# Kernel tuning notes

Measured on AMD Instinct MI355X. Metric: run time of the kernel, lower is better.

Reference implementation:

```python
import jax, jax.numpy as jnp
import numpy as np

B, S, H = 2, 2048, 2048
NH, G = 16, 4
HD = H // NH          # 128
REP = NH // G         # 4 query heads per KV group
KV = G * HD           # 512


def setup_inputs() -> dict:
    key = jax.random.key(0)
    ks = jax.random.split(key, 10)
    s = 0.02
    X = jax.random.normal(ks[0], (B, S, H), dtype=jnp.float32)
    Wq = jax.random.normal(ks[1], (H, H), dtype=jnp.float32) * s
    bq = jnp.zeros((H,), dtype=jnp.float32)
    Wk = jax.random.normal(ks[2], (H, KV), dtype=jnp.float32) * s
    bk = jnp.zeros((KV,), dtype=jnp.float32)
    Wv = jax.random.normal(ks[3], (H, KV), dtype=jnp.float32) * s
    bv = jnp.zeros((KV,), dtype=jnp.float32)
    Wo = jax.random.normal(ks[4], (H, H), dtype=jnp.float32) * s
    bo = jnp.zeros((H,), dtype=jnp.float32)
    # causal mask: 1 where attention is disallowed (strict upper triangle)
    casual_mask = jnp.triu(jnp.ones((S, S), dtype=jnp.float32), k=1)[None, None]
    return {"X": X, "Wq": Wq, "bq": bq, "Wk": Wk, "bk": bk,
            "Wv": Wv, "bv": bv, "Wo": Wo, "bo": bo,
            "casual_mask": casual_mask}


def reference(X, Wq, bq, Wk, bk, Wv, bv, Wo, bo, casual_mask):
    # projections
    q = X @ Wq + bq                          # [B,S,H]
    k = X @ Wk + bk                          # [B,S,G*HD]
    v = X @ Wv + bv                          # [B,S,G*HD]
    # split heads; q grouped as (group, rep) to match torch expand ordering
    q = q.reshape(B, S, NH, HD).transpose(0, 2, 1, 3)       # [B,NH,S,HD]
    q = q.reshape(B, G, REP, S, HD)                          # [B,G,REP,S,HD]
    k = k.reshape(B, S, G, HD).transpose(0, 2, 1, 3)         # [B,G,S,HD]
    v = v.reshape(B, S, G, HD).transpose(0, 2, 1, 3)         # [B,G,S,HD]
    scale = 1.0 / jnp.sqrt(jnp.float32(HD))
    scores = jnp.einsum('bgrqd,bgkd->bgrqk', q, k) * scale   # [B,G,REP,S,S]
    scores = scores + casual_mask * (-1e9)
    probs = jax.nn.softmax(scores, axis=-1)
    out = jnp.einsum('bgrqk,bgkd->bgrqd', probs, v)          # [B,G,REP,S,HD]
    out = out.reshape(B, NH, S, HD).transpose(0, 2, 1, 3).reshape(B, S, H)
    return out @ Wo + bo
```

## Files before the change

### kernel.cpp

```cpp
#include <hip/hip_runtime.h>

#define B_   2
#define S_   2048
#define H_   2048
#define NH_  16
#define G_   4
#define HD_  128
#define KV_  512
#define HQKV 3072

typedef __attribute__((ext_vector_type(8))) short bf16x8;
typedef __attribute__((ext_vector_type(4))) float f32x4;

__device__ __forceinline__ unsigned short f2bf(float f) {
    unsigned u = __float_as_uint(f);
    u += 0x7fff + ((u >> 16) & 1);
    return (unsigned short)(u >> 16);
}
__device__ __forceinline__ float bf2f(unsigned short s) {
    return __uint_as_float(((unsigned)s) << 16);
}
__device__ __forceinline__ unsigned cvtpk(float a, float b) {
    unsigned r;
    asm volatile("v_cvt_pk_bf16_f32 %0, %1, %2" : "=v"(r) : "v"(a), "v"(b));
    return r;
}

#define GLDS16(gsrc, ldst)                                                            \
    __builtin_amdgcn_global_load_lds(                                                 \
        (const __attribute__((address_space(1))) void*)(gsrc),                        \
        (__attribute__((address_space(3))) void*)(ldst), 16, 0, 0)

#define SC2F (0.08838834764831843f * 1.4426950408889634f)

__global__ void k_cvt_bf16(const float* __restrict__ in, unsigned short* __restrict__ out, int n4) {
    int i = blockIdx.x * blockDim.x + threadIdx.x;
    if (i >= n4) return;
    float4 v = ((const float4*)in)[i];
    ushort4 o;
    o.x = f2bf(v.x); o.y = f2bf(v.y); o.z = f2bf(v.z); o.w = f2bf(v.w);
    ((ushort4*)out)[i] = o;
}

__global__ void k_transpose_cvt(const float* __restrict__ in, unsigned short* __restrict__ out,
                                int R, int C) {
    __shared__ float t[32][33];
    int c0 = blockIdx.x * 32, r0 = blockIdx.y * 32;
    int tx = threadIdx.x, ty = threadIdx.y;
#pragma unroll
    for (int i = 0; i < 4; ++i)
        t[ty + i*8][tx] = in[(size_t)(r0 + ty + i*8) * C + c0 + tx];
    __syncthreads();
#pragma unroll
    for (int i = 0; i < 4; ++i)
        out[(size_t)(c0 + ty + i*8) * R + r0 + tx] = f2bf(t[tx][ty + i*8]);
}

__global__ void k_transpose_qkv(const float* __restrict__ Wq, const float* __restrict__ Wk,
                                const float* __restrict__ Wv, unsigned short* __restrict__ out) {
    __shared__ float t[32][33];
    int n0g = blockIdx.x * 32;
    int h0 = blockIdx.y * 32;
    const float* src; int C, n0l;
    if (n0g < H_)            { src = Wq; C = H_;  n0l = n0g; }
    else if (n0g < H_ + KV_) { src = Wk; C = KV_; n0l = n0g - H_; }
    else                     { src = Wv; C = KV_; n0l = n0g - H_ - KV_; }
    int tx = threadIdx.x, ty = threadIdx.y;
#pragma unroll
    for (int i = 0; i < 4; ++i)
        t[ty + i*8][tx] = src[(size_t)(h0 + ty + i*8) * C + n0l + tx];
    __syncthreads();
#pragma unroll
    for (int i = 0; i < 4; ++i)
        out[(size_t)(n0g + ty + i*8) * H_ + h0 + tx] = f2bf(t[tx][ty + i*8]);
}

__global__ void k_concat_bias(const float* __restrict__ bq, const float* __restrict__ bk,
                              const float* __restrict__ bv, float* __restrict__ out) {
    int i = blockIdx.x * 256 + threadIdx.x;
    if (i >= HQKV) return;
    out[i] = (i < H_) ? bq[i] : (i < H_ + KV_ ? bk[i - H_] : bv[i - H_ - KV_]);
}

__global__ void k_transpose_v(const unsigned short* __restrict__ in, unsigned short* __restrict__ out) {
    __shared__ unsigned short t[32][33];
    int b = blockIdx.z;
    int c0 = blockIdx.x * 32, s0 = blockIdx.y * 32;
    int tx = threadIdx.x, ty = threadIdx.y;
#pragma unroll
    for (int i = 0; i < 4; ++i)
        t[ty + i*8][tx] = in[((size_t)b * S_ + s0 + ty + i*8) * HQKV + (H_ + KV_) + c0 + tx];
    __syncthreads();
#pragma unroll
    for (int i = 0; i < 4; ++i)
        out[((size_t)b * KV_ + c0 + ty + i*8) * S_ + s0 + tx] = t[tx][ty + i*8];
}

template <bool BF16OUT, bool QSCALE>
__global__ __launch_bounds__(256) void k_gemm_bt(
    const unsigned short* __restrict__ A, const unsigned short* __restrict__ Bt,
    const float* __restrict__ bias, void* __restrict__ Cout, int M, int N, int K) {
    __shared__ __align__(16) unsigned short As[128 * 64];
    __shared__ __align__(16) unsigned short Bs[128 * 64];
    const int tid = threadIdx.x, lane = tid & 63, w = tid >> 6;
    const int l15 = lane & 15, l4 = lane >> 4;
    const int wr = w >> 1, wc = w & 1;
    const int m0 = blockIdx.x * 128, n0 = blockIdx.y * 128;
    f32x4 acc[4][4] = {};

    for (int kt = 0; kt < K; kt += 64) {
        __syncthreads();
#pragma unroll
        for (int i = 0; i < 4; ++i) {
            int p = (w * 4 + i) * 64 + lane;
            int row = p >> 3, c = (p & 7) ^ (row & 7);
            GLDS16(A + (size_t)(m0 + row) * K + kt + c * 8, As + (size_t)(w * 4 + i) * 512);
        }
#pragma unroll
        for (int i = 0; i < 4; ++i) {
            int p = (w * 4 + i) * 64 + lane;
            int row = p >> 3, c = (p & 7) ^ (row & 7);
            GLDS16(Bt + (size_t)(n0 + row) * K + kt + c * 8, Bs + (size_t)(w * 4 + i) * 512);
        }
        __syncthreads();
#pragma unroll
        for (int ks = 0; ks < 2; ++ks) {
            bf16x8 af[4], bfr[4];
#pragma unroll
            for (int m = 0; m < 4; ++m) {
                int row = wr * 64 + m * 16 + l15;
                int ch = (ks * 4 + l4) ^ (row & 7);
                af[m] = *(const bf16x8*)(As + row * 64 + ch * 8);
            }
#pragma unroll
            for (int n = 0; n < 4; ++n) {
                int row = wc * 64 + n * 16 + l15;
                int ch = (ks * 4 + l4) ^ (row & 7);
                bfr[n] = *(const bf16x8*)(Bs + row * 64 + ch * 8);
            }
#pragma unroll
            for (int m = 0; m < 4; ++m)
#pragma unroll
                for (int n = 0; n < 4; ++n)
                    acc[m][n] = __builtin_amdgcn_mfma_f32_16x16x32_bf16(af[m], bfr[n], acc[m][n], 0, 0, 0);
        }
    }
#pragma unroll
    for (int m = 0; m < 4; ++m) {
        int row = m0 + wr * 64 + m * 16 + l4 * 4;
#pragma unroll
        for (int n = 0; n < 4; ++n) {
            int col = n0 + wc * 64 + n * 16 + l15;
            float bv = bias[col];
#pragma unroll
            for (int r = 0; r < 4; ++r) {
                float v = acc[m][n][r] + bv;
                if (QSCALE) { if (col < H_) v *= SC2F; }
                if (BF16OUT)
                    ((unsigned short*)Cout)[(size_t)(row + r) * N + col] = f2bf(v);
                else
                    ((float*)Cout)[(size_t)(row + r) * N + col] = v;
            }
        }
    }
}

__global__ __launch_bounds__(256, 4) void k_flash(
    const unsigned short* __restrict__ QKV,
    const unsigned short* __restrict__ VT,
    unsigned short* __restrict__ Oa,
    unsigned short* __restrict__ part1,
    float* __restrict__ mlbuf) {
    __shared__ __align__(16) unsigned short Ks[64 * 128];
    __shared__ __align__(16) unsigned short Vs[128 * 64];
    const int tid = threadIdx.x, lane = tid & 63, w = tid >> 6;
    const int l15 = lane & 15, l4 = lane >> 4;
    const int bid = blockIdx.x;
    const int xcd = bid & 7, idx = bid >> 3;
    const int bh = xcd * 4 + (idx & 3);
    const int jidx = idx >> 2;
    const int b = bh >> 4, nh = bh & 15, g = nh >> 2;

    int qt, t0, t1, mode;
    if (jidx < 16) { qt = 16 + jidx; t0 = 0; t1 = 16; mode = 1; }
    else {
        int k = jidx - 16, j = k >> 1;
        if ((k & 1) == 0) { qt = 31 - j; t0 = 16; t1 = qt + 1; mode = 2; }
        else              { qt = 15 - j; t0 = 0;  t1 = qt + 1; mode = 0; }
    }
    const int qbase = qt * 64 + w * 16;

    const unsigned short* kgbase = QKV + (size_t)b * S_ * HQKV + H_ + g * HD_;
    const unsigned short* vgbase = VT + ((size_t)b * KV_ + g * HD_) * S_;

    auto issueK = [&](int kt) {
        const int kv0 = kt * 64;
#pragma unroll
        for (int i = 0; i < 4; ++i) {
            int p = i * 256 + tid;
            int row = p >> 4, c = (p & 15) ^ (row & 15);
            GLDS16(kgbase + (size_t)(kv0 + row) * HQKV + c * 8, &Ks[(i * 256 + w * 64) * 8]);
        }
    };
    auto issueV = [&](int kt) {
        const int kv0 = kt * 64;
#pragma unroll
        for (int i = 0; i < 4; ++i) {
            int p = i * 256 + tid;
            int row = p >> 3, c = (p & 7) ^ (row & 7);
            GLDS16(vgbase + (size_t)row * S_ + kv0 + c * 8, &Vs[(i * 256 + w * 64) * 8]);
        }
    };

    bf16x8 qf[4];
#pragma unroll
    for (int kb = 0; kb < 4; ++kb)
        qf[kb] = *(const bf16x8*)(QKV + (size_t)(b * S_ + qbase + l15) * HQKV +
                                  nh * HD_ + kb * 32 + l4 * 8);

    f32x4 o[8] = {};
    float m_r = -1e30f, l_r = 0.f;

    const int src0 = l15 + 16 * ((2 * l4) & 3);
    const int src1 = l15 + 16 * ((2 * l4 + 1) & 3);
    const bool hsel = ((l4 >> 1) & 1) != 0;

    issueK(t0);
    issueV(t0);

    for (int kt = t0; kt < t1; ++kt) {
        const int kv0 = kt * 64;
        asm volatile("s_waitcnt vmcnt(4)" ::: "memory");
        __builtin_amdgcn_s_barrier();
        __builtin_amdgcn_sched_barrier(0);

        f32x4 s[4] = {};
#pragma unroll
        for (int kb = 0; kb < 4; ++kb) {
            bf16x8 kf[4];
#pragma unroll
            for (int n = 0; n < 4; ++n) {
                int row = n * 16 + l15;
                int sl = (kb * 4 + l4) ^ (row & 15);
                kf[n] = *(const bf16x8*)(&Ks[(row * 16 + sl) * 8]);
            }
            __builtin_amdgcn_s_setprio(1);
#pragma unroll
            for (int n = 0; n < 4; ++n)
                s[n] = __builtin_amdgcn_mfma_f32_16x16x32_bf16(kf[n], qf[kb], s[n], 0, 0, 0);
            __builtin_amdgcn_s_setprio(0);
        }
        if (kv0 + 63 > qbase) {
            const int qrow = qbase + l15;
#pragma unroll
            for (int n = 0; n < 4; ++n)
#pragma unroll
                for (int r = 0; r < 4; ++r) {
                    int kcol = kv0 + n * 16 + l4 * 4 + r;
                    if (kcol > qrow) s[n][r] = -1e30f;
                }
        }
        float pmax = s[0][0];
#pragma unroll
        for (int n = 0; n < 4; ++n)
#pragma unroll
            for (int r = 0; r < 4; ++r) pmax = fmaxf(pmax, s[n][r]);
        pmax = fmaxf(pmax, __shfl_xor(pmax, 16));
        pmax = fmaxf(pmax, __shfl_xor(pmax, 32));
        if (__any(pmax > m_r + 8.0f)) {
            float mn = fmaxf(m_r, pmax);
            float sf = exp2f(m_r - mn);
            m_r = mn;
            l_r *= sf;
#pragma unroll
            for (int nc = 0; nc < 8; ++nc) {
                f32x4 t = o[nc];
                t[0] *= sf; t[1] *= sf; t[2] *= sf; t[3] *= sf;
                o[nc] = t;
            }
        }
        float rsum = 0.f;
#pragma unroll
        for (int n = 0; n < 4; ++n)
#pragma unroll
            for (int r = 0; r < 4; ++r) {
                float p = exp2f(s[n][r] - m_r);
                s[n][r] = p;
                rsum += p;
            }
        rsum += __shfl_xor(rsum, 16);
        rsum += __shfl_xor(rsum, 32);
        l_r += rsum;

        unsigned plo[4], phi[4];
#pragma unroll
        for (int n = 0; n < 4; ++n) {
            plo[n] = cvtpk(s[n][0], s[n][1]);
            phi[n] = cvtpk(s[n][2], s[n][3]);
        }

        asm volatile("s_waitcnt vmcnt(0)" ::: "memory");
        __builtin_amdgcn_s_barrier();
        __builtin_amdgcn_sched_barrier(0);
        if (kt + 1 < t1) issueK(kt + 1);

#pragma unroll
        for (int kb = 0; kb < 2; ++kb) {
            const int n0i = 2 * kb, n1i = 2 * kb + 1;
            unsigned a0, a1, w0, w1, w2, w3;
            a0 = __shfl((int)plo[n0i], src0); a1 = __shfl((int)plo[n1i], src0); w0 = hsel ? a1 : a0;
            a0 = __shfl((int)phi[n0i], src0); a1 = __shfl((int)phi[n1i], src0); w1 = hsel ? a1 : a0;
            a0 = __shfl((int)plo[n0i], src1); a1 = __shfl((int)plo[n1i], src1); w2 = hsel ? a1 : a0;
            a0 = __shfl((int)phi[n0i], src1); a1 = __shfl((int)phi[n1i], src1); w3 = hsel ? a1 : a0;
            int4 pw = make_int4((int)w0, (int)w1, (int)w2, (int)w3);
            bf16x8 pf = *(bf16x8*)&pw;
            __builtin_amdgcn_s_setprio(1);
#pragma unroll
            for (int nc = 0; nc < 8; ++nc) {
                int row = nc * 16 + l15;
                int sl = (kb * 4 + l4) ^ (row & 7);
                bf16x8 vf = *(const bf16x8*)(&Vs[(row * 8 + sl) * 8]);
                o[nc] = __builtin_amdgcn_mfma_f32_16x16x32_bf16(vf, pf, o[nc], 0, 0, 0);
            }
            __builtin_amdgcn_s_setprio(0);
        }

        __builtin_amdgcn_s_barrier();
        __builtin_amdgcn_sched_barrier(0);
        if (kt + 1 < t1) issueV(kt + 1);
    }

    const int qrow = qbase + l15;
    if (mode == 0) {
        float inv = 1.0f / l_r;
        size_t base = (size_t)(b * S_ + qrow) * H_ + nh * HD_ + l4 * 4;
#pragma unroll
        for (int nc = 0; nc < 8; ++nc) {
            uint2 pk;
            pk.x = cvtpk(o[nc][0] * inv, o[nc][1] * inv);
            pk.y = cvtpk(o[nc][2] * inv, o[nc][3] * inv);
            *(uint2*)(Oa + base + nc * 16) = pk;
        }
    } else {
        const int base = bh * 16 + (qt - 16);
        const int c = (mode == 1) ? 0 : 1;
        float* mlrec = mlbuf + (size_t)(base * 2 + c) * 64 * 2;
        if (l4 == 0) {
            int row = w * 16 + l15;
            mlrec[row * 2 + 0] = m_r;
            mlrec[row * 2 + 1] = l_r;
        }
        if (mode == 1) {
            size_t ob = (size_t)(b * S_ + qrow) * H_ + nh * HD_ + l4 * 4;
#pragma unroll
            for (int nc = 0; nc < 8; ++nc) {
                uint2 pk;
                pk.x = cvtpk(o[nc][0], o[nc][1]);
                pk.y = cvtpk(o[nc][2], o[nc][3]);
                *(uint2*)(Oa + ob + nc * 16) = pk;
            }
        } else {
            size_t pb = ((size_t)base * 64 + w * 16 + l15) * 128 + l4 * 4;
#pragma unroll
            for (int nc = 0; nc < 8; ++nc) {
                uint2 pk;
                pk.x = cvtpk(o[nc][0], o[nc][1]);
                pk.y = cvtpk(o[nc][2], o[nc][3]);
                *(uint2*)(part1 + pb + nc * 16) = pk;
            }
        }
    }
}

__global__ __launch_bounds__(256) void k_combine(
    const float* __restrict__ mlbuf, const unsigned short* __restrict__ part1,
    unsigned short* __restrict__ Oa) {
    int rec = blockIdx.x;
    int bh = rec >> 4, qt = 16 + (rec & 15);
    int b = bh >> 4, nh = bh & 15;
    int row = threadIdx.x >> 2;
    int dseg = (threadIdx.x & 3) * 32;
    const float* ml0 = mlbuf + (size_t)(rec * 2 + 0) * 128;
    const float* ml1 = mlbuf + (size_t)(rec * 2 + 1) * 128;
    float m0 = ml0[row * 2], l0 = ml0[row * 2 + 1];
    float m1 = ml1[row * 2], l1 = ml1[row * 2 + 1];
    float M = fmaxf(m0, m1);
    float a0 = exp2f(m0 - M), a1 = exp2f(m1 - M);
    float L = a0 * l0 + a1 * l1;
    float s0 = a0 / L, s1 = a1 / L;
    size_t ob = ((size_t)(b * S_) + qt * 64 + row) * H_ + nh * HD_ + dseg;
    const unsigned short* p1 = part1 + ((size_t)rec * 64 + row) * 128 + dseg;
#pragma unroll
    for (int i = 0; i < 4; ++i) {
        bf16x8 v0 = *(const bf16x8*)(Oa + ob + i * 8);
        bf16x8 v1 = *(const bf16x8*)(p1 + i * 8);
        bf16x8 oo;
#pragma unroll
        for (int e = 0; e < 8; ++e)
            oo[e] = (short)f2bf(bf2f((unsigned short)v0[e]) * s0 +
                                bf2f((unsigned short)v1[e]) * s1);
        *(bf16x8*)(Oa + ob + i * 8) = oo;
    }
}

extern "C" void kernel_launch(void* const* d_in, const int* in_sizes, int n_in,
                              void* d_out, int out_size, void* d_ws, size_t ws_size,
                              hipStream_t stream) {
    const float* X  = (const float*)d_in[0];
    const float* Wq = (const float*)d_in[1];
    const float* bq = (const float*)d_in[2];
    const float* Wk = (const float*)d_in[3];
    const float* bk = (const float*)d_in[4];
    const float* Wv = (const float*)d_in[5];
    const float* bv = (const float*)d_in[6];
    const float* Wo = (const float*)d_in[7];
    const float* bo = (const float*)d_in[8];
    float* out = (float*)d_out;

    if (ws_size < 80000000) return;
    char* ws = (char*)d_ws;
    unsigned short* Xb    = (unsigned short*)(ws);
    unsigned short* WqkvT = (unsigned short*)(ws + 16777216);
    unsigned short* WoT   = (unsigned short*)(ws + 29360128);
    unsigned short* QKV   = (unsigned short*)(ws + 37748736);
    unsigned short* VbT   = (unsigned short*)(ws + 62914560);
    unsigned short* part1 = (unsigned short*)(ws + 67108864);
    float*          mlbuf = (float*)(ws + 75497472);
    float*          bqkv  = (float*)(ws + 76021760);
    unsigned short* AOb   = Xb;

    k_cvt_bf16<<<(B_ * S_ * H_ / 4 + 255) / 256, 256, 0, stream>>>(X, Xb, B_ * S_ * H_ / 4);
    k_transpose_qkv<<<dim3(HQKV / 32, H_ / 32), dim3(32, 8), 0, stream>>>(Wq, Wk, Wv, WqkvT);
    k_transpose_cvt<<<dim3(H_ / 32, H_ / 32), dim3(32, 8), 0, stream>>>(Wo, WoT, H_, H_);
    k_concat_bias<<<(HQKV + 255) / 256, 256, 0, stream>>>(bq, bk, bv, bqkv);

    k_gemm_bt<true, true><<<dim3(32, 24), 256, 0, stream>>>(Xb, WqkvT, bqkv, QKV, 4096, HQKV, 2048);

    k_transpose_v<<<dim3(KV_ / 32, S_ / 32, B_), dim3(32, 8), 0, stream>>>(QKV, VbT);
    k_flash<<<dim3(1536), 256, 0, stream>>>(QKV, VbT, AOb, part1, mlbuf);
    k_combine<<<dim3(512), 256, 0, stream>>>(mlbuf, part1, AOb);

    k_gemm_bt<false, false><<<dim3(32, 16), 256, 0, stream>>>(AOb, WoT, bo, out, 4096, 2048, 2048);
}
```

Baseline: 221.3 us.

## Double-buffer GEMM LDS tiles with prefetch and XCD-aware block remap

Result: no change. 223.5 us (+1.0%).

```diff
diff --git a/kernel.cpp b/kernel.cpp
--- a/kernel.cpp
+++ b/kernel.cpp
@@ -99,62 +99,86 @@
 template <bool BF16OUT, bool QSCALE>
 __global__ __launch_bounds__(256) void k_gemm_bt(
     const unsigned short* __restrict__ A, const unsigned short* __restrict__ Bt,
-    const float* __restrict__ bias, void* __restrict__ Cout, int M, int N, int K) {
-    __shared__ __align__(16) unsigned short As[128 * 64];
-    __shared__ __align__(16) unsigned short Bs[128 * 64];
+    const float* __restrict__ bias, void* __restrict__ Cout, int M, int N, int K, int nbx) {
+    __shared__ __align__(16) unsigned short As[2][128 * 64];
+    __shared__ __align__(16) unsigned short Bs[2][128 * 64];
     const int tid = threadIdx.x, lane = tid & 63, w = tid >> 6;
     const int l15 = lane & 15, l4 = lane >> 4;
     const int wr = w >> 1, wc = w & 1;
-    const int m0 = blockIdx.x * 128, n0 = blockIdx.y * 128;
+    const int nwg = nbx * ((gridDim.x) / nbx);
+    const int cpx = gridDim.x >> 3;
+    const int wg = (blockIdx.x & 7) * cpx + (blockIdx.x >> 3);
+    const int m0 = (wg % nbx) * 128, n0 = (wg / nbx) * 128;
+    (void)nwg;
     f32x4 acc[4][4] = {};
 
-    for (int kt = 0; kt < K; kt += 64) {
-        __syncthreads();
+    auto stage = [&](int buf, int kt) {
 #pragma unroll
         for (int i = 0; i < 4; ++i) {
             int p = (w * 4 + i) * 64 + lane;
             int row = p >> 3, c = (p & 7) ^ (row & 7);
-            GLDS16(A + (size_t)(m0 + row) * K + kt + c * 8, As + (size_t)(w * 4 + i) * 512);
+            GLDS16(A + (size_t)(m0 + row) * K + kt * 64 + c * 8,
+                   &As[buf][(w * 4 + i) * 512]);
         }
 #pragma unroll
         for (int i = 0; i < 4; ++i) {
             int p = (w * 4 + i) * 64 + lane;
             int row = p >> 3, c = (p & 7) ^ (row & 7);
-            GLDS16(Bt + (size_t)(n0 + row) * K + kt + c * 8, Bs + (size_t)(w * 4 + i) * 512);
-        }
-        __syncthreads();
-#pragma unroll
-        for (int ks = 0; ks < 2; ++ks) {
-            bf16x8 af[4], bfr[4];
-#pragma unroll
-            for (int m = 0; m < 4; ++m) {
-                int row = wr * 64 + m * 16 + l15;
-                int ch = (ks * 4 + l4) ^ (row & 7);
-                af[m] = *(const bf16x8*)(As + row * 64 + ch * 8);
-            }
+            GLDS16(Bt + (size_t)(n0 + row) * K + kt * 64 + c * 8,
+                   &Bs[buf][(w * 4 + i) * 512]);
+        }
+    };
+
+    const int NT = K >> 6;
+    stage(0, 0);
+    if (NT > 1) stage(1, 1);
+
+    for (int t = 0; t < NT; ++t) {
+        const int cur = t & 1;
+        if (t + 1 < NT) { asm volatile("s_waitcnt vmcnt(8)" ::: "memory"); }
+        else            { asm volatile("s_waitcnt vmcnt(0)" ::: "memory"); }
+        __builtin_amdgcn_s_barrier();
+        __builtin_amdgcn_sched_barrier(0);
+
+        bf16x8 bfr[2][4];
+#pragma unroll
+        for (int ks = 0; ks < 2; ++ks)
 #pragma unroll
             for (int n = 0; n < 4; ++n) {
                 int row = wc * 64 + n * 16 + l15;
-                int ch = (ks * 4 + l4) ^ (row & 7);
-                bfr[n] = *(const bf16x8*)(Bs + row * 64 + ch * 8);
-            }
-#pragma unroll
-            for (int m = 0; m < 4; ++m)
-#pragma unroll
-                for (int n = 0; n < 4; ++n)
-                    acc[m][n] = __builtin_amdgcn_mfma_f32_16x16x32_bf16(af[m], bfr[n], acc[m][n], 0, 0, 0);
-        }
-    }
-#pragma unroll
-    for (int m = 0; m < 4; ++m) {
-        int row = m0 + wr * 64 + m * 16 + l4 * 4;
+                int sl = (ks * 4 + l4) ^ (row & 7);
+                bfr[ks][n] = *(const bf16x8*)(&Bs[cur][(row * 8 + sl) * 8]);
+            }
+#pragma unroll
+        for (int fr = 0; fr < 4; ++fr) {
+            int row = wr * 64 + fr * 16 + l15;
+            bf16x8 af0 = *(const bf16x8*)(&As[cur][(row * 8 + (l4 ^ (row & 7))) * 8]);
+            bf16x8 af1 = *(const bf16x8*)(&As[cur][(row * 8 + ((4 + l4) ^ (row & 7))) * 8]);
+            __builtin_amdgcn_s_setprio(1);
+#pragma unroll
+            for (int n = 0; n < 4; ++n)
+                acc[fr][n] = __builtin_amdgcn_mfma_f32_16x16x32_bf16(af0, bfr[0][n], acc[fr][n], 0, 0, 0);
+#pragma unroll
+            for (int n = 0; n < 4; ++n)
+                acc[fr][n] = __builtin_amdgcn_mfma_f32_16x16x32_bf16(af1, bfr[1][n], acc[fr][n], 0, 0, 0);
+            __builtin_amdgcn_s_setprio(0);
+        }
+
+        __builtin_amdgcn_s_barrier();
+        __builtin_amdgcn_sched_barrier(0);
+        if (t + 2 < NT) stage(cur, t + 2);
+    }
+
+#pragma unroll
+    for (int fr = 0; fr < 4; ++fr) {
+        int row = m0 + wr * 64 + fr * 16 + l4 * 4;
 #pragma unroll
         for (int n = 0; n < 4; ++n) {
             int col = n0 + wc * 64 + n * 16 + l15;
             float bv = bias[col];
 #pragma unroll
             for (int r = 0; r < 4; ++r) {
-                float v = acc[m][n][r] + bv;
+                float v = acc[fr][n][r] + bv;
                 if (QSCALE) { if (col < H_) v *= SC2F; }
                 if (BF16OUT)
                     ((unsigned short*)Cout)[(size_t)(row + r) * N + col] = f2bf(v);
@@ -434,11 +458,11 @@
     k_transpose_cvt<<<dim3(H_ / 32, H_ / 32), dim3(32, 8), 0, stream>>>(Wo, WoT, H_, H_);
     k_concat_bias<<<(HQKV + 255) / 256, 256, 0, stream>>>(bq, bk, bv, bqkv);
 
-    k_gemm_bt<true, true><<<dim3(32, 24), 256, 0, stream>>>(Xb, WqkvT, bqkv, QKV, 4096, HQKV, 2048);
+    k_gemm_bt<true, true><<<dim3(32 * 24), 256, 0, stream>>>(Xb, WqkvT, bqkv, QKV, 4096, HQKV, 2048, 32);
 
     k_transpose_v<<<dim3(KV_ / 32, S_ / 32, B_), dim3(32, 8), 0, stream>>>(QKV, VbT);
     k_flash<<<dim3(1536), 256, 0, stream>>>(QKV, VbT, AOb, part1, mlbuf);
     k_combine<<<dim3(512), 256, 0, stream>>>(mlbuf, part1, AOb);
 
-    k_gemm_bt<false, false><<<dim3(32, 16), 256, 0, stream>>>(AOb, WoT, bo, out, 4096, 2048, 2048);
-}
+    k_gemm_bt<false, false><<<dim3(32 * 16), 256, 0, stream>>>(AOb, WoT, bo, out, 4096, 2048, 2048, 32);
+}
```

## Use 256x256 double-buffered pipelined GEMM kernel for the QKV projection

Applied to the files above, without the earlier changes.

After: 208.2 us. -5.9%, faster.

```diff
diff --git a/kernel.cpp b/kernel.cpp
--- a/kernel.cpp
+++ b/kernel.cpp
@@ -94,6 +94,121 @@
 #pragma unroll
     for (int i = 0; i < 4; ++i)
         out[((size_t)b * KV_ + c0 + ty + i*8) * S_ + s0 + tx] = t[tx][ty + i*8];
+}
+
+template <bool BF16OUT, bool QSCALE>
+__global__ __launch_bounds__(512, 2) void k_gemm256(
+    const unsigned short* __restrict__ A, const unsigned short* __restrict__ Bt,
+    const float* __restrict__ bias, void* __restrict__ Cout, int M, int N, int K) {
+    __shared__ __align__(16) unsigned short As[2][256 * 64];
+    __shared__ __align__(16) unsigned short Bs[2][256 * 64];
+    const int tid = threadIdx.x, lane = tid & 63;
+    const int w = tid >> 6;
+    const int l15 = lane & 15, l4 = lane >> 4;
+    const int wr = w >> 2, wc = w & 3;
+    const int m0 = blockIdx.x * 256, n0 = blockIdx.y * 256;
+    f32x4 acc[8][4] = {};
+
+    auto stageA = [&](int buf, int kt, int h) {
+#pragma unroll
+        for (int i = 0; i < 2; ++i) {
+            int p = i * 512 + tid;
+            int j = p >> 3;
+            int row = h * 64 + (j >> 6) * 128 + (j & 63);
+            int sc = p & 7;
+            int c = sc ^ (row & 7);
+            GLDS16(A + (size_t)(m0 + row) * K + kt * 64 + c * 8,
+                   &As[buf][(row * 8 + sc) * 8]);
+        }
+    };
+    auto stageB = [&](int buf, int kt, int h) {
+#pragma unroll
+        for (int i = 0; i < 2; ++i) {
+            int p = i * 512 + tid;
+            int j = p >> 3;
+            int row = h * 32 + (j >> 5) * 64 + (j & 31);
+            int sc = p & 7;
+            int c = sc ^ (row & 7);
+            GLDS16(Bt + (size_t)(n0 + row) * K + kt * 64 + c * 8,
+                   &Bs[buf][(row * 8 + sc) * 8]);
+        }
+    };
+
+    const int NT = K >> 6;
+    stageB(0, 0, 0); stageA(0, 0, 0); stageB(0, 0, 1); stageA(0, 0, 1);
+    stageB(1, 1, 0); stageA(1, 1, 0);
+
+    bf16x8 bf[2][2];
+    for (int t = 0; t < NT; ++t) {
+        const int cur = t & 1, nxt = cur ^ 1;
+        if (t == NT - 1) { asm volatile("s_waitcnt vmcnt(0)" ::: "memory"); }
+        else             { asm volatile("s_waitcnt vmcnt(4)" ::: "memory"); }
+        __builtin_amdgcn_s_barrier();
+        __builtin_amdgcn_sched_barrier(0);
+
+#pragma unroll
+        for (int q = 0; q < 4; ++q) {
+            const int nh = q >> 1, mh = q & 1;
+            bf16x8 af[4][2];
+#pragma unroll
+            for (int mf2 = 0; mf2 < 4; ++mf2)
+#pragma unroll
+                for (int ks = 0; ks < 2; ++ks) {
+                    int row = wr * 128 + (mh * 4 + mf2) * 16 + l15;
+                    int ch = (ks * 4 + l4) ^ (row & 7);
+                    af[mf2][ks] = *(const bf16x8*)(&As[cur][(row * 8 + ch) * 8]);
+                }
+            if (mh == 0) {
+#pragma unroll
+                for (int nf2 = 0; nf2 < 2; ++nf2)
+#pragma unroll
+                    for (int ks = 0; ks < 2; ++ks) {
+                        int row = wc * 64 + (nh * 2 + nf2) * 16 + l15;
+                        int ch = (ks * 4 + l4) ^ (row & 7);
+                        bf[nf2][ks] = *(const bf16x8*)(&Bs[cur][(row * 8 + ch) * 8]);
+                    }
+            }
+            if (q == 0)      { if (t + 1 < NT) stageB(nxt, t + 1, 1); }
+            else if (q == 1) { if (t + 1 < NT) stageA(nxt, t + 1, 1); }
+            else if (q == 2) { if (t + 2 < NT) stageB(cur, t + 2, 0); }
+            else             { if (t + 2 < NT) stageA(cur, t + 2, 0); }
+
+            __builtin_amdgcn_sched_barrier(0);
+            __builtin_amdgcn_s_barrier();
+            asm volatile("s_waitcnt lgkmcnt(0)" ::: "memory");
+            __builtin_amdgcn_sched_barrier(0);
+            __builtin_amdgcn_s_setprio(1);
+#pragma unroll
+            for (int mf2 = 0; mf2 < 4; ++mf2)
+#pragma unroll
+                for (int nf2 = 0; nf2 < 2; ++nf2)
+#pragma unroll
+                    for (int ks = 0; ks < 2; ++ks)
+                        acc[mh * 4 + mf2][nh * 2 + nf2] = __builtin_amdgcn_mfma_f32_16x16x32_bf16(
+                            af[mf2][ks], bf[nf2][ks], acc[mh * 4 + mf2][nh * 2 + nf2], 0, 0, 0);
+            __builtin_amdgcn_s_setprio(0);
+            __builtin_amdgcn_s_barrier();
+        }
+    }
+
+#pragma unroll
+    for (int mf = 0; mf < 8; ++mf) {
+        int row = m0 + wr * 128 + mf * 16 + l4 * 4;
+#pragma unroll
+        for (int nf = 0; nf < 4; ++nf) {
+            int col = n0 + wc * 64 + nf * 16 + l15;
+            float bv = bias[col];
+#pragma unroll
+            for (int r = 0; r < 4; ++r) {
+                float v = acc[mf][nf][r] + bv;
+                if (QSCALE) { if (col < H_) v *= SC2F; }
+                if (BF16OUT)
+                    ((unsigned short*)Cout)[(size_t)(row + r) * N + col] = f2bf(v);
+                else
+                    ((float*)Cout)[(size_t)(row + r) * N + col] = v;
+            }
+        }
+    }
 }
 
 template <bool BF16OUT, bool QSCALE>
@@ -434,7 +549,7 @@
     k_transpose_cvt<<<dim3(H_ / 32, H_ / 32), dim3(32, 8), 0, stream>>>(Wo, WoT, H_, H_);
     k_concat_bias<<<(HQKV + 255) / 256, 256, 0, stream>>>(bq, bk, bv, bqkv);
 
-    k_gemm_bt<true, true><<<dim3(32, 24), 256, 0, stream>>>(Xb, WqkvT, bqkv, QKV, 4096, HQKV, 2048);
+    k_gemm256<true, true><<<dim3(16, 12), 512, 0, stream>>>(Xb, WqkvT, bqkv, QKV, 4096, HQKV, 2048);
 
     k_transpose_v<<<dim3(KV_ / 32, S_ / 32, B_), dim3(32, 8), 0, stream>>>(QKV, VbT);
     k_flash<<<dim3(1536), 256, 0, stream>>>(QKV, VbT, AOb, part1, mlbuf);
```
